# Kernel optimization log

Measured on AMD Instinct MI355X. Metric: run time of the kernel, lower is better.

Reference implementation:

```python
import jax, jax.numpy as jnp
import numpy as np

B, N, D = 16, 512, 256
HEADS = 8
HIDEF = 1024
BLOCK, WINDOW = 32, 64
LEVELS = 5
PYOUT = 128
NCLS, NANCH = 5, 9
NEG = -1e9


def _sinusoidal_pos(n, d):
    # PositionEmbeddingStatic: deterministic sinusoidal table [n, d]
    pos = np.arange(n)[:, None].astype(np.float64)
    i = np.arange(d)[None, :]
    angle = pos / np.power(10000.0, (2 * (i // 2)) / d)
    pe = np.where(i % 2 == 0, np.sin(angle), np.cos(angle))
    return jnp.asarray(pe, jnp.float32)


def _layernorm(x, g, b, eps=1e-5):
    m = x.mean(-1, keepdims=True)
    v = x.var(-1, keepdims=True)
    return (x - m) * jax.lax.rsqrt(v + eps) * g + b


def _bn(x_bcn, g, b, eps=1e-5):
    # BatchNorm1d in training mode: per-channel batch stats over (B, N)
    m = x_bcn.mean((0, 2), keepdims=True)
    v = x_bcn.var((0, 2), keepdims=True)
    return (x_bcn - m) * jax.lax.rsqrt(v + eps) * g[None, :, None] + b[None, :, None]


def _sparse_attention(x, Wqkv, bqkv, Wo, bo):
    # Windowed block-sparse attention: queries in block i attend to key blocks
    # [i-w, i+w] with w = window_size // block_size. Never materializes SxS.
    Bx, Nx, Dx = x.shape
    H, dh = HEADS, Dx // HEADS
    nb, bs = Nx // BLOCK, BLOCK
    w = WINDOW // BLOCK
    qkv = x @ Wqkv + bqkv
    q, k, v = jnp.split(qkv, 3, axis=-1)

    def to_blocks(t):  # [B,N,D] -> [B,H,nb,bs,dh]
        return t.reshape(Bx, nb, bs, H, dh).transpose(0, 3, 1, 2, 4)

    q, k, v = to_blocks(q), to_blocks(k), to_blocks(v)
    offs = list(range(-w, w + 1))
    # roll by -o puts key block (i+o) at query-block position i
    k_band = jnp.concatenate([jnp.roll(k, -o, axis=2) for o in offs], axis=3)
    v_band = jnp.concatenate([jnp.roll(v, -o, axis=2) for o in offs], axis=3)
    blk = jnp.arange(nb)
    valid = jnp.concatenate(
        [jnp.repeat(((blk + o >= 0) & (blk + o < nb))[:, None], bs, axis=1) for o in offs],
        axis=1)  # [nb, (2w+1)*bs]
    scale = 1.0 / jnp.sqrt(jnp.asarray(dh, x.dtype))
    scores = jnp.einsum('bhnqd,bhnkd->bhnqk', q, k_band) * scale
    scores = jnp.where(valid[None, None, :, None, :], scores, NEG)
    p = jax.nn.softmax(scores, axis=-1)
    o = jnp.einsum('bhnqk,bhnkd->bhnqd', p, v_band)
    o = o.transpose(0, 2, 3, 1, 4).reshape(Bx, Nx, Dx)
    return o @ Wo + bo


def setup_inputs():
    key = jax.random.key(0)
    ks = iter(jax.random.split(key, 48))
    g = lambda shape, s=0.02: jax.random.normal(next(ks), shape, jnp.float32) * s
    z = lambda *shape: jnp.zeros(shape, jnp.float32)
    o = lambda *shape: jnp.ones(shape, jnp.float32)
    return {
        'x': jax.random.normal(next(ks), (B, N, D), jnp.float32),
        'patch_W': g((D, D)), 'patch_b': z(D),
        'ln_g': o(D), 'ln_b': z(D),
        'ff_W1': g((D, HIDEF)), 'ff_b1': z(HIDEF),
        'ff_W2': g((HIDEF, D)), 'ff_b2': z(D),
        'Wqkv': g((D, 3 * D)), 'bqkv': z(3 * D),
        'Wo': g((D, D)), 'bo': z(D),
        'bn1_g': o(D), 'bn1_b': z(D),
        'bn2_g': o(D), 'bn2_b': z(D),
        'pyr_W': g((LEVELS, D, PYOUT)), 'pyr_b': z(LEVELS, PYOUT),
        'fcl_W': g((LEVELS * PYOUT * N, 128), 0.005), 'fcl_b': z(128),
        'addbn_g': o(128), 'addbn_b': z(128),
        'cls_W1': g((128, 256)), 'cls_b1': z(256),
        'cls_W2': g((256, NCLS * NANCH)), 'cls_b2': z(NCLS * NANCH),
        'box_W1': g((128, 128)), 'box_b1': z(128),
        'box_W2': g((128, 4 * NANCH)), 'box_b2': z(4 * NANCH),
    }


def reference(x, patch_W, patch_b, ln_g, ln_b, ff_W1, ff_b1, ff_W2, ff_b2,
              Wqkv, bqkv, Wo, bo, bn1_g, bn1_b, bn2_g, bn2_b,
              pyr_W, pyr_b, fcl_W, fcl_b, addbn_g, addbn_b,
              cls_W1, cls_b1, cls_W2, cls_b2, box_W1, box_b1, box_W2, box_b2):
    pos = _sinusoidal_pos(N, D)

    def ff(h):
        return jax.nn.gelu(h @ ff_W1 + ff_b1) @ ff_W2 + ff_b2

    def mnt(h):
        h = _layernorm(h @ patch_W + patch_b, ln_g, ln_b)  # patch embed + norm
        h = h + pos[None]
        idt = h
        h = ff(h)
        h = _sparse_attention(h, Wqkv, bqkv, Wo, bo)
        h = h + idt
        h = _bn(h.transpose(0, 2, 1), bn1_g, bn1_b).transpose(0, 2, 1)
        idt = h
        h = ff(h) + idt
        h = _bn(h.transpose(0, 2, 1), bn2_g, bn2_b).transpose(0, 2, 1)
        return h

    outs = []
    for _ in range(5):
        x = mnt(x)
        outs.append(x.transpose(0, 2, 1))  # [B, D, N]

    # pyramid: per-level 1x1 conv D -> 128
    feats = [jnp.einsum('bdn,dc->bcn', outs[i], pyr_W[i]) + pyr_b[i][None, :, None]
             for i in range(LEVELS)]
    flat = jnp.concatenate([f.reshape(f.shape[0], -1) for f in feats], axis=1)
    add = (flat @ fcl_W + fcl_b)[:, :, None]          # [B,128,1]
    add = _bn(add, addbn_g, addbn_b).transpose(0, 2, 1)  # [B,1,128]
    cls = jax.nn.relu(add @ cls_W1 + cls_b1) @ cls_W2 + cls_b2
    cls = jax.nn.softmax(cls, axis=-1).reshape(-1, NANCH, NCLS)  # eval mode softmax
    box = (jax.nn.relu(add @ box_W1 + box_b1) @ box_W2 + box_b2).reshape(-1, NANCH, 4)
    return jnp.concatenate([cls, box], axis=-1)  # [B, NANCH, NCLS+4]
```

## Files before the change

### kernel.cpp

```cpp
#include <hip/hip_runtime.h>
#include <hip/hip_bf16.h>
#include <math.h>

#define B_ 16
#define N_ 512
#define D_ 256
#define HEADS_ 8
#define DH_ 32
#define HIDEF_ 1024
#define NBLK_ 16
#define BS_ 32
#define LEVELS_ 5
#define PYOUT_ 128
#define ROWS_ (B_ * N_)
#define FCL_K 327680
#define FCL_KB 256
#define FCL_CHUNKS 1280

typedef __attribute__((ext_vector_type(8))) short short8;
typedef __attribute__((ext_vector_type(4))) short short4v;
typedef __attribute__((ext_vector_type(4))) unsigned short ushort4v;
typedef __attribute__((ext_vector_type(4))) float f32x4;

__device__ __forceinline__ float bf2f(short u) {
    return __uint_as_float(((unsigned int)(unsigned short)u) << 16);
}
__device__ __forceinline__ unsigned short f2bf(float x) {
    __hip_bfloat16 h = __float2bfloat16(x);
    return *reinterpret_cast<unsigned short*>(&h);
}

__global__ void pos_kernel(float* __restrict__ pos) {
    int idx = blockIdx.x * 256 + threadIdx.x;
    if (idx >= N_ * D_) return;
    int n = idx >> 8, i = idx & 255;
    double angle = (double)n / pow(10000.0, (double)(2 * (i >> 1)) / 256.0);
    pos[idx] = (float)((i & 1) ? cos(angle) : sin(angle));
}

__device__ __forceinline__ float gelu_f(float x) {
    float x3 = x * x * x;
    return 0.5f * x * (1.f + tanhf(0.7978845608028654f * (x + 0.044715f * x3)));
}

__global__ void tobf16_kernel(const float* __restrict__ x, __hip_bfloat16* __restrict__ y, int n) {
    int i = blockIdx.x * 256 + threadIdx.x;
    if (i < n) y[i] = __float2bfloat16(x[i]);
}

__global__ __launch_bounds__(256) void wconv_kernel(const float* __restrict__ W,
                                                    __hip_bfloat16* __restrict__ Wt,
                                                    int K, int N) {
    int z = blockIdx.z;
    const float* Wz = W + (size_t)z * K * N;
    __hip_bfloat16* Wtz = Wt + (size_t)z * K * N;
    __shared__ float t[32][33];
    int bx = blockIdx.x * 32, by = blockIdx.y * 32;
    int tx = threadIdx.x, ty = threadIdx.y;
#pragma unroll
    for (int i = 0; i < 32; i += 8)
        t[ty + i][tx] = Wz[(size_t)(by + ty + i) * N + bx + tx];
    __syncthreads();
#pragma unroll
    for (int i = 0; i < 32; i += 8)
        Wtz[(size_t)(bx + ty + i) * K + by + tx] = __float2bfloat16(t[tx][ty + i]);
}

template <int ACT, bool OUTF, bool OUTB, bool SCAT, bool STATS, int BN>
__global__ __launch_bounds__(256) void bgemm_kernel(
    const __hip_bfloat16* __restrict__ A, const __hip_bfloat16* __restrict__ Wt,
    const float* __restrict__ bias, const float* __restrict__ resid,
    float* __restrict__ C, __hip_bfloat16* __restrict__ Cb, int M, int Nn, int K,
    int level, float* __restrict__ bnp) {
    __shared__ __hip_bfloat16 Alds[128 * 32];
    __shared__ __hip_bfloat16 Blds[BN * 32];
    constexpr int MW = (BN == 128) ? 4 : 2;
    constexpr int WH = (BN == 128) ? 64 : 32;
    constexpr int BR = BN / 64;
    int tid = threadIdx.x;
    int wid = tid >> 6, lane = tid & 63;
    int row0 = blockIdx.y * 128, col0 = blockIdx.x * BN;
    int wr = (BN == 128) ? (wid >> 1) : wid;
    int wc = (BN == 128) ? (wid & 1) : 0;
    int r16 = lane & 15, kq = lane >> 4;
    int rdoff = kq ^ ((r16 >> 1) & 3);

    f32x4 acc[MW][4];
#pragma unroll
    for (int m = 0; m < MW; m++)
#pragma unroll
        for (int n = 0; n < 4; n++) acc[m][n] = (f32x4){0.f, 0.f, 0.f, 0.f};

    for (int k0 = 0; k0 < K; k0 += 32) {
#pragma unroll
        for (int i = 0; i < 2; i++) {
            int slot = i * 256 + tid;
            int row = slot >> 2, qp = slot & 3;
            int q = qp ^ ((row >> 1) & 3);
            const __hip_bfloat16* ga = A + (size_t)(row0 + row) * K + k0 + q * 8;
            __builtin_amdgcn_global_load_lds(
                (const __attribute__((address_space(1))) void*)ga,
                (__attribute__((address_space(3))) void*)((char*)Alds + i * 4096 + wid * 1024),
                16, 0, 0);
        }
#pragma unroll
        for (int i = 0; i < BR; i++) {
            int slot = i * 256 + tid;
            int row = slot >> 2, qp = slot & 3;
            int q = qp ^ ((row >> 1) & 3);
            const __hip_bfloat16* gb = Wt + (size_t)(col0 + row) * K + k0 + q * 8;
            __builtin_amdgcn_global_load_lds(
                (const __attribute__((address_space(1))) void*)gb,
                (__attribute__((address_space(3))) void*)((char*)Blds + i * 4096 + wid * 1024),
                16, 0, 0);
        }
        __syncthreads();
        short8 af[MW], bf[4];
#pragma unroll
        for (int m = 0; m < MW; m++) {
            int row = wr * WH + m * 16 + r16;
            af[m] = *reinterpret_cast<const short8*>(
                reinterpret_cast<const char*>(Alds) + row * 64 + rdoff * 16);
        }
#pragma unroll
        for (int n = 0; n < 4; n++) {
            int row = wc * 64 + n * 16 + r16;
            bf[n] = *reinterpret_cast<const short8*>(
                reinterpret_cast<const char*>(Blds) + row * 64 + rdoff * 16);
        }
#pragma unroll
        for (int m = 0; m < MW; m++)
#pragma unroll
            for (int n = 0; n < 4; n++)
                acc[m][n] = __builtin_amdgcn_mfma_f32_16x16x32_bf16(af[m], bf[n], acc[m][n], 0, 0, 0);
        __syncthreads();
    }

    int rg = lane >> 4;
    float s1a[4] = {0.f, 0.f, 0.f, 0.f}, s2a[4] = {0.f, 0.f, 0.f, 0.f};
    if (SCAT) {
#pragma unroll
        for (int n = 0; n < 4; n++) {
            int cc = col0 + wc * 64 + n * 16 + r16;
            int bb = cc >> 9, nn = cc & 511;
            float* dst = C + (size_t)bb * (LEVELS_ * PYOUT_ * N_) +
                         (size_t)level * PYOUT_ * N_ + nn;
#pragma unroll
            for (int m = 0; m < MW; m++) {
                int rbase = wr * WH + m * 16 + rg * 4;
#pragma unroll
                for (int j = 0; j < 4; j++) {
                    int ch = rbase + j;
                    dst[(size_t)ch * N_] = acc[m][n][j] + bias[ch];
                }
            }
        }
    } else {
#pragma unroll
        for (int n = 0; n < 4; n++) {
            int cc = col0 + wc * 64 + n * 16 + r16;
            float bv = bias[cc];
#pragma unroll
            for (int m = 0; m < MW; m++) {
                int rb = row0 + wr * WH + m * 16 + rg * 4;
#pragma unroll
                for (int j = 0; j < 4; j++) {
                    int r = rb + j;
                    float v = acc[m][n][j] + bv;
                    if (resid) v += resid[(size_t)r * Nn + cc];
                    if (ACT == 1) v = gelu_f(v);
                    if (OUTF) C[(size_t)r * Nn + cc] = v;
                    if (OUTB) Cb[(size_t)r * Nn + cc] = __float2bfloat16(v);
                    if (STATS) { s1a[n] += v; s2a[n] += v * v; }
                }
            }
        }
    }
    if (STATS) {
        float* sc = (float*)Alds;
        int part = wid * 4 + rg;
#pragma unroll
        for (int n = 0; n < 4; n++) {
            int c = wc * 64 + n * 16 + r16;
            sc[c * 16 + part] = s1a[n];
            sc[1024 + c * 16 + part] = s2a[n];
        }
        __syncthreads();
        if (tid < BN) {
            float a = 0.f, b2 = 0.f;
#pragma unroll
            for (int p = 0; p < 16; p++) {
                a += sc[tid * 16 + p];
                b2 += sc[1024 + tid * 16 + p];
            }
            bnp[blockIdx.y * 256 + col0 + tid] = a;
            bnp[16384 + blockIdx.y * 256 + col0 + tid] = b2;
        }
    }
}

__global__ __launch_bounds__(256) void ln_pos_kernel(
    const float* __restrict__ t, const float* __restrict__ g,
    const float* __restrict__ b, const float* __restrict__ pos,
    float* __restrict__ h, __hip_bfloat16* __restrict__ hb) {
    int lane = threadIdx.x & 63;
    int row = blockIdx.x * 4 + (threadIdx.x >> 6);
    const float4* xr = (const float4*)(t + (size_t)row * D_);
    float4 v = xr[lane];
    float s = v.x + v.y + v.z + v.w;
#pragma unroll
    for (int mk = 32; mk; mk >>= 1) s += __shfl_xor(s, mk);
    float mean = s * (1.f / 256.f);
    float dx = v.x - mean, dy = v.y - mean, dz = v.z - mean, dw = v.w - mean;
    float q = dx * dx + dy * dy + dz * dz + dw * dw;
#pragma unroll
    for (int mk = 32; mk; mk >>= 1) q += __shfl_xor(q, mk);
    float rstd = rsqrtf(q * (1.f / 256.f) + 1e-5f);
    float4 g4 = ((const float4*)g)[lane];
    float4 b4 = ((const float4*)b)[lane];
    float4 p4 = ((const float4*)pos)[(size_t)(row & (N_ - 1)) * 64 + lane];
    float o0 = dx * rstd * g4.x + b4.x + p4.x;
    float o1 = dy * rstd * g4.y + b4.y + p4.y;
    float o2 = dz * rstd * g4.z + b4.z + p4.z;
    float o3 = dw * rstd * g4.w + b4.w + p4.w;
    ((float4*)(h + (size_t)row * D_))[lane] = (float4){o0, o1, o2, o3};
    ushort4v u = {f2bf(o0), f2bf(o1), f2bf(o2), f2bf(o3)};
    *((ushort4v*)(hb + (size_t)row * D_) + lane) = u;
}

__global__ __launch_bounds__(256) void bn_finish_kernel(
    const float* __restrict__ bnp, float* __restrict__ stats) {
    int c = threadIdx.x;
    float s = 0.f, s2 = 0.f;
#pragma unroll 4
    for (int y = 0; y < 64; y++) {
        s += bnp[y * 256 + c];
        s2 += bnp[16384 + y * 256 + c];
    }
    float m = s * (1.f / 8192.f);
    stats[c] = m;
    stats[D_ + c] = s2 * (1.f / 8192.f) - m * m;
}

__global__ __launch_bounds__(256) void bn_apply_kernel(
    const float* __restrict__ x, const float* __restrict__ stats,
    const float* __restrict__ g, const float* __restrict__ b,
    float* __restrict__ y, __hip_bfloat16* __restrict__ yb) {
    int lane = threadIdx.x & 63;
    int row = blockIdx.x * 4 + (threadIdx.x >> 6);
    float4 m4 = ((const float4*)stats)[lane];
    float4 v4 = ((const float4*)(stats + D_))[lane];
    float4 g4 = ((const float4*)g)[lane];
    float4 b4 = ((const float4*)b)[lane];
    float4 x4 = ((const float4*)(x + (size_t)row * D_))[lane];
    float o0 = (x4.x - m4.x) * rsqrtf(v4.x + 1e-5f) * g4.x + b4.x;
    float o1 = (x4.y - m4.y) * rsqrtf(v4.y + 1e-5f) * g4.y + b4.y;
    float o2 = (x4.z - m4.z) * rsqrtf(v4.z + 1e-5f) * g4.z + b4.z;
    float o3 = (x4.w - m4.w) * rsqrtf(v4.w + 1e-5f) * g4.w + b4.w;
    if (y) ((float4*)(y + (size_t)row * D_))[lane] = (float4){o0, o1, o2, o3};
    if (yb) {
        ushort4v u = {f2bf(o0), f2bf(o1), f2bf(o2), f2bf(o3)};
        *((ushort4v*)(yb + (size_t)row * D_) + lane) = u;
    }
}

__global__ __launch_bounds__(256) void attn_kernel(
    const __hip_bfloat16* __restrict__ qkv, __hip_bfloat16* __restrict__ outb) {
    int bx = blockIdx.x, h = blockIdx.y, b = blockIdx.z;
    int tid = threadIdx.x;
    int wid = tid >> 6, lane = tid & 63;
    __shared__ __hip_bfloat16 Klds[256 * 32];
    __shared__ __hip_bfloat16 Vt[32 * 264];
    const short* q16 = (const short*)qkv;

#pragma unroll
    for (int r = 0; r < 4; r++) {
        int slot = r * 256 + tid;
        int row = slot >> 2, qp = slot & 3;
        int ql = qp ^ ((row >> 1) & 3);
        int jb = bx * 4 - 2 + (row >> 5);
        jb = jb < 0 ? 0 : (jb > 15 ? 15 : jb);
        const short* ga = q16 + ((size_t)(b * N_ + jb * 32 + (row & 31))) * 768 + 256 + h * 32 + ql * 8;
        __builtin_amdgcn_global_load_lds(
            (const __attribute__((address_space(1))) void*)ga,
            (__attribute__((address_space(3))) void*)((char*)Klds + r * 4096 + wid * 1024),
            16, 0, 0);
    }
    {
        int row = tid;
        int jb = bx * 4 - 2 + (row >> 5);
        jb = jb < 0 ? 0 : (jb > 15 ? 15 : jb);
        const short* gv = q16 + ((size_t)(b * N_ + jb * 32 + (row & 31))) * 768 + 512 + h * 32;
        short8 v0 = *(const short8*)(gv);
        short8 v1 = *(const short8*)(gv + 8);
        short8 v2 = *(const short8*)(gv + 16);
        short8 v3 = *(const short8*)(gv + 24);
        short* vt = (short*)Vt;
#pragma unroll
        for (int e = 0; e < 8; e++) {
            vt[(e) * 264 + row] = v0[e];
            vt[(8 + e) * 264 + row] = v1[e];
            vt[(16 + e) * 264 + row] = v2[e];
            vt[(24 + e) * 264 + row] = v3[e];
        }
    }
    __syncthreads();

    int i = bx * 4 + wid;
    int c = lane & 15, g = lane >> 4;
    const float scale = 0.17677669529663687f;

#pragma unroll
    for (int qt = 0; qt < 2; qt++) {
        const short* qa = q16 + ((size_t)(b * N_ + i * 32 + qt * 16 + c)) * 768 + h * 32 + g * 8;
        short8 bq = *(const short8*)qa;
        f32x4 st[10];
#pragma unroll
        for (int t = 0; t < 10; t++) {
            int jb = i - 2 + (t >> 1);
            if (jb >= 0 && jb < NBLK_) {
                int row = wid * 32 + t * 16 + c;
                int phys = g ^ ((row >> 1) & 3);
                short8 ak = *(const short8*)((const char*)Klds + row * 64 + phys * 16);
                st[t] = __builtin_amdgcn_mfma_f32_16x16x32_bf16(
                    ak, bq, (f32x4){0.f, 0.f, 0.f, 0.f}, 0, 0, 0);
            }
        }
        float mx = -1e30f;
#pragma unroll
        for (int t = 0; t < 10; t++) {
            int jb = i - 2 + (t >> 1);
            if (jb >= 0 && jb < NBLK_) {
#pragma unroll
                for (int j = 0; j < 4; j++) {
                    st[t][j] *= scale;
                    mx = fmaxf(mx, st[t][j]);
                }
            }
        }
        mx = fmaxf(mx, __shfl_xor(mx, 16));
        mx = fmaxf(mx, __shfl_xor(mx, 32));
        float sum = 0.f;
#pragma unroll
        for (int t = 0; t < 10; t++) {
            int jb = i - 2 + (t >> 1);
            if (jb >= 0 && jb < NBLK_) {
#pragma unroll
                for (int j = 0; j < 4; j++) {
                    float e = __expf(st[t][j] - mx);
                    st[t][j] = e;
                    sum += e;
                }
            }
        }
        sum += __shfl_xor(sum, 16);
        sum += __shfl_xor(sum, 32);
        float inv = 1.f / sum;
        f32x4 o0 = (f32x4){0.f, 0.f, 0.f, 0.f};
        f32x4 o1 = (f32x4){0.f, 0.f, 0.f, 0.f};
        const short* vt = (const short*)Vt;
#pragma unroll
        for (int t = 0; t < 10; t++) {
            int jb = i - 2 + (t >> 1);
            if (jb >= 0 && jb < NBLK_) {
                short8 pa = (short8)0;
#pragma unroll
                for (int j = 0; j < 4; j++) pa[j] = (short)f2bf(st[t][j] * inv);
                int kb = wid * 32 + t * 16 + g * 4;
                short4v vb0 = *(const short4v*)(vt + (0 * 16 + c) * 264 + kb);
                short4v vb1 = *(const short4v*)(vt + (1 * 16 + c) * 264 + kb);
                short8 b0 = (short8)0, b1 = (short8)0;
#pragma unroll
                for (int e = 0; e < 4; e++) { b0[e] = vb0[e]; b1[e] = vb1[e]; }
                o0 = __builtin_amdgcn_mfma_f32_16x16x32_bf16(pa, b0, o0, 0, 0, 0);
                o1 = __builtin_amdgcn_mfma_f32_16x16x32_bf16(pa, b1, o1, 0, 0, 0);
            }
        }
#pragma unroll
        for (int j = 0; j < 4; j++) {
            size_t rbase = ((size_t)(b * N_ + i * 32 + qt * 16 + g * 4 + j)) * D_ + h * DH_;
            outb[rbase + c] = __float2bfloat16(o0[j]);
            outb[rbase + 16 + c] = __float2bfloat16(o1[j]);
        }
    }
}

__global__ __launch_bounds__(256) void fcl_partial_kernel(
    const float* __restrict__ flat, const float* __restrict__ W,
    float* __restrict__ partial) {
    int chunk = blockIdx.x;
    int t = threadIdx.x;
    int k0 = chunk * FCL_KB;
    __shared__ float fl[FCL_KB][18];
#pragma unroll
    for (int b = 0; b < 16; b++)
        fl[t][b] = flat[(size_t)b * FCL_K + k0 + t];
    __syncthreads();
    int jq = t & 31, bg = t >> 5;
    f32x4 acc0 = (f32x4){0.f, 0.f, 0.f, 0.f};
    f32x4 acc1 = (f32x4){0.f, 0.f, 0.f, 0.f};
    const f32x4* W4 = (const f32x4*)W;
#pragma unroll 8
    for (int k = 0; k < FCL_KB; k++) {
        f32x4 wv = W4[(size_t)(k0 + k) * 32 + jq];
        float2 f2 = *(const float2*)&fl[k][bg * 2];
        acc0 += wv * f2.x;
        acc1 += wv * f2.y;
    }
    *(f32x4*)&partial[((size_t)chunk * 16 + bg * 2 + 0) * 128 + jq * 4] = acc0;
    *(f32x4*)&partial[((size_t)chunk * 16 + bg * 2 + 1) * 128 + jq * 4] = acc1;
}

__global__ __launch_bounds__(256) void fcl_reduce_kernel(
    const float* __restrict__ partial, const float* __restrict__ fcl_b,
    float* __restrict__ add) {
    int c0 = blockIdx.x * 32;
    int t = threadIdx.x;
    int ry = t >> 5, cx = t & 31;
    float s = 0.f;
    for (int r = ry; r < FCL_CHUNKS; r += 8)
        s += partial[(size_t)r * 2048 + c0 + cx];
    __shared__ float red[8][32];
    red[ry][cx] = s; __syncthreads();
    if (ry == 0) {
        float tot = 0.f;
#pragma unroll
        for (int q = 0; q < 8; q++) tot += red[q][cx];
        int col = c0 + cx;
        add[col] = tot + fcl_b[col & 127];
    }
}

__global__ __launch_bounds__(256) void head_kernel(
    const float* __restrict__ add, const float* __restrict__ abg, const float* __restrict__ abb,
    const float* __restrict__ cls_W1, const float* __restrict__ cls_b1,
    const float* __restrict__ cls_W2, const float* __restrict__ cls_b2,
    const float* __restrict__ box_W1, const float* __restrict__ box_b1,
    const float* __restrict__ box_W2, const float* __restrict__ box_b2,
    float* __restrict__ out) {
    __shared__ float a2[16][128];
    __shared__ float cm[16][256];
    __shared__ float cls[16][45];
    __shared__ float bmid[16][128];
    __shared__ float smden[16];
    int t = threadIdx.x;
    if (t < 128) {
        float m = 0.f;
#pragma unroll
        for (int b = 0; b < 16; b++) m += add[b * 128 + t];
        m *= (1.f / 16.f);
        float v = 0.f;
#pragma unroll
        for (int b = 0; b < 16; b++) { float d = add[b * 128 + t] - m; v += d * d; }
        v *= (1.f / 16.f);
        float sc = rsqrtf(v + 1e-5f) * abg[t];
#pragma unroll
        for (int b = 0; b < 16; b++) a2[b][t] = (add[b * 128 + t] - m) * sc + abb[t];
    }
    __syncthreads();
    for (int idx = t; idx < 4096; idx += 256) {
        int m = idx >> 8, c = idx & 255;
        float a = cls_b1[c];
        for (int k = 0; k < 128; k++) a += a2[m][k] * cls_W1[k * 256 + c];
        cm[m][c] = fmaxf(a, 0.f);
    }
    for (int idx = t; idx < 2048; idx += 256) {
        int m = idx >> 7, c = idx & 127;
        float a = box_b1[c];
        for (int k = 0; k < 128; k++) a += a2[m][k] * box_W1[k * 128 + c];
        bmid[m][c] = fmaxf(a, 0.f);
    }
    __syncthreads();
    for (int idx = t; idx < 720; idx += 256) {
        int m = idx / 45, c = idx % 45;
        float a = cls_b2[c];
        for (int k = 0; k < 256; k++) a += cm[m][k] * cls_W2[k * 45 + c];
        cls[m][c] = a;
    }
    __syncthreads();
    if (t < 16) {
        float mx = -1e30f;
        for (int c = 0; c < 45; c++) mx = fmaxf(mx, cls[t][c]);
        float s = 0.f;
        for (int c = 0; c < 45; c++) { float e = expf(cls[t][c] - mx); cls[t][c] = e; s += e; }
        smden[t] = s;
    }
    for (int idx = t; idx < 576; idx += 256) {
        int m = idx / 36, c = idx % 36;
        float a = box_b2[c];
        for (int k = 0; k < 128; k++) a += bmid[m][k] * box_W2[k * 36 + c];
        out[m * 81 + (c >> 2) * 9 + 5 + (c & 3)] = a;
    }
    __syncthreads();
    for (int idx = t; idx < 720; idx += 256) {
        int m = idx / 45, c = idx % 45;
        out[m * 81 + (c / 5) * 9 + (c % 5)] = cls[m][c] / smden[m];
    }
}

extern "C" void kernel_launch(void* const* d_in, const int* in_sizes, int n_in,
                              void* d_out, int out_size, void* d_ws, size_t ws_size,
                              hipStream_t stream) {
    const float* x_in    = (const float*)d_in[0];
    const float* patch_W = (const float*)d_in[1];
    const float* patch_b = (const float*)d_in[2];
    const float* ln_g    = (const float*)d_in[3];
    const float* ln_b    = (const float*)d_in[4];
    const float* ff_W1   = (const float*)d_in[5];
    const float* ff_b1   = (const float*)d_in[6];
    const float* ff_W2   = (const float*)d_in[7];
    const float* ff_b2   = (const float*)d_in[8];
    const float* Wqkv    = (const float*)d_in[9];
    const float* bqkv    = (const float*)d_in[10];
    const float* Wo      = (const float*)d_in[11];
    const float* bo      = (const float*)d_in[12];
    const float* bn1_g   = (const float*)d_in[13];
    const float* bn1_b   = (const float*)d_in[14];
    const float* bn2_g   = (const float*)d_in[15];
    const float* bn2_b   = (const float*)d_in[16];
    const float* pyr_W   = (const float*)d_in[17];
    const float* pyr_b   = (const float*)d_in[18];
    const float* fcl_W   = (const float*)d_in[19];
    const float* fcl_b   = (const float*)d_in[20];
    const float* addbn_g = (const float*)d_in[21];
    const float* addbn_b = (const float*)d_in[22];
    const float* cls_W1  = (const float*)d_in[23];
    const float* cls_b1  = (const float*)d_in[24];
    const float* cls_W2  = (const float*)d_in[25];
    const float* cls_b2  = (const float*)d_in[26];
    const float* box_W1  = (const float*)d_in[27];
    const float* box_b1  = (const float*)d_in[28];
    const float* box_W2  = (const float*)d_in[29];
    const float* box_b2  = (const float*)d_in[30];
    float* out = (float*)d_out;

    float* ws = (float*)d_ws;
    size_t off = 0;
    float* POS   = ws + off; off += 131072;
    float* H     = ws + off; off += 2097152;
    float* T     = ws + off; off += 2097152;
    float* UNION = ws + off; off += 4194304;
    float* FLAT  = ws + off; off += 5242880;
    float* PART  = ws + off; off += (size_t)FCL_CHUNKS * 2048;
    float* STATS = ws + off; off += 512;
    float* BNP   = ws + off; off += 2 * 64 * 256;
    float* ADD   = ws + off; off += 2048;
    __hip_bfloat16* Hb   = (__hip_bfloat16*)(ws + off); off += 1048576;
    __hip_bfloat16* Tb   = (__hip_bfloat16*)(ws + off); off += 1048576;
    __hip_bfloat16* Xb   = (__hip_bfloat16*)(ws + off); off += 1048576;
    __hip_bfloat16* ATb  = (__hip_bfloat16*)(ws + off); off += 1048576;
    __hip_bfloat16* patchWt = (__hip_bfloat16*)(ws + off); off += 32768;
    __hip_bfloat16* qkvWt   = (__hip_bfloat16*)(ws + off); off += 98304;
    __hip_bfloat16* WoWt    = (__hip_bfloat16*)(ws + off); off += 32768;
    __hip_bfloat16* W1t     = (__hip_bfloat16*)(ws + off); off += 131072;
    __hip_bfloat16* W2t     = (__hip_bfloat16*)(ws + off); off += 131072;
    __hip_bfloat16* pyrWt   = (__hip_bfloat16*)(ws + off); off += 81920;
    __hip_bfloat16* MIDb = (__hip_bfloat16*)UNION;
    __hip_bfloat16* QKVb = (__hip_bfloat16*)UNION;

    pos_kernel<<<(N_ * D_ + 255) / 256, 256, 0, stream>>>(POS);
    wconv_kernel<<<dim3(D_ / 32, D_ / 32, 1), dim3(32, 8), 0, stream>>>(patch_W, patchWt, D_, D_);
    wconv_kernel<<<dim3(768 / 32, D_ / 32, 1), dim3(32, 8), 0, stream>>>(Wqkv, qkvWt, D_, 768);
    wconv_kernel<<<dim3(D_ / 32, D_ / 32, 1), dim3(32, 8), 0, stream>>>(Wo, WoWt, D_, D_);
    wconv_kernel<<<dim3(HIDEF_ / 32, D_ / 32, 1), dim3(32, 8), 0, stream>>>(ff_W1, W1t, D_, HIDEF_);
    wconv_kernel<<<dim3(D_ / 32, HIDEF_ / 32, 1), dim3(32, 8), 0, stream>>>(ff_W2, W2t, HIDEF_, D_);
    wconv_kernel<<<dim3(PYOUT_ / 32, D_ / 32, LEVELS_), dim3(32, 8), 0, stream>>>(pyr_W, pyrWt, D_, PYOUT_);
    tobf16_kernel<<<(ROWS_ * D_ + 255) / 256, 256, 0, stream>>>(x_in, Xb, ROWS_ * D_);

    for (int it = 0; it < 5; it++) {
        bgemm_kernel<0, true, false, false, false, 64><<<dim3(4, 64), 256, 0, stream>>>(
            Xb, patchWt, patch_b, nullptr, T, nullptr, ROWS_, D_, D_, 0, nullptr);
        ln_pos_kernel<<<ROWS_ / 4, 256, 0, stream>>>(T, ln_g, ln_b, POS, H, Hb);
        bgemm_kernel<1, false, true, false, false, 128><<<dim3(8, 64), 256, 0, stream>>>(
            Hb, W1t, ff_b1, nullptr, nullptr, MIDb, ROWS_, HIDEF_, D_, 0, nullptr);
        bgemm_kernel<0, false, true, false, false, 64><<<dim3(4, 64), 256, 0, stream>>>(
            MIDb, W2t, ff_b2, nullptr, nullptr, Tb, ROWS_, D_, HIDEF_, 0, nullptr);
        bgemm_kernel<0, false, true, false, false, 128><<<dim3(6, 64), 256, 0, stream>>>(
            Tb, qkvWt, bqkv, nullptr, nullptr, QKVb, ROWS_, 768, D_, 0, nullptr);
        attn_kernel<<<dim3(4, HEADS_, B_), 256, 0, stream>>>(QKVb, ATb);
        bgemm_kernel<0, true, false, false, true, 64><<<dim3(4, 64), 256, 0, stream>>>(
            ATb, WoWt, bo, H, T, nullptr, ROWS_, D_, D_, 0, BNP);
        bn_finish_kernel<<<1, 256, 0, stream>>>(BNP, STATS);
        bn_apply_kernel<<<ROWS_ / 4, 256, 0, stream>>>(T, STATS, bn1_g, bn1_b, H, Hb);
        bgemm_kernel<1, false, true, false, false, 128><<<dim3(8, 64), 256, 0, stream>>>(
            Hb, W1t, ff_b1, nullptr, nullptr, MIDb, ROWS_, HIDEF_, D_, 0, nullptr);
        bgemm_kernel<0, true, false, false, true, 64><<<dim3(4, 64), 256, 0, stream>>>(
            MIDb, W2t, ff_b2, H, T, nullptr, ROWS_, D_, HIDEF_, 0, BNP);
        bn_finish_kernel<<<1, 256, 0, stream>>>(BNP, STATS);
        bn_apply_kernel<<<ROWS_ / 4, 256, 0, stream>>>(T, STATS, bn2_g, bn2_b, nullptr, Xb);
        bgemm_kernel<0, false, false, true, false, 64><<<dim3(128, 1), 256, 0, stream>>>(
            pyrWt + (size_t)it * D_ * PYOUT_, Xb, pyr_b + it * PYOUT_, nullptr,
            FLAT, nullptr, PYOUT_, ROWS_, D_, it, nullptr);
    }

    fcl_partial_kernel<<<FCL_CHUNKS, 256, 0, stream>>>(FLAT, fcl_W, PART);
    fcl_reduce_kernel<<<64, 256, 0, stream>>>(PART, fcl_b, ADD);
    head_kernel<<<1, 256, 0, stream>>>(ADD, addbn_g, addbn_b,
        cls_W1, cls_b1, cls_W2, cls_b2, box_W1, box_b1, box_W2, box_b2, out);
    (void)in_sizes; (void)n_in; (void)out_size; (void)ws_size;
}
```

Before: 1.035 ms.

## Fuse patch GEMM with LayerNorm, fold BN finish into apply, retile FCL partial

A new kernel computes the patch-embedding GEMM for 32-row tiles with MFMA, stages the output in LDS, and applies LayerNorm plus the positional add in place. This removes the fp32 round trip of T and one launch per iteration. BN stat finishing is merged into the apply kernel: each of 256 blocks recomputes the column stats from the partials and then normalizes 32 rows, which removes two launches per iteration at the cost of redundant stat reads. The FCL partial kernel is remapped so each thread handles one output column for 8 batches, using scalar weight loads and float4 LDS reads.

```diff
diff --git a/kernel.cpp b/kernel.cpp
--- a/kernel.cpp
+++ b/kernel.cpp
@@ -199,68 +199,144 @@
     }
 }
 
-__global__ __launch_bounds__(256) void ln_pos_kernel(
-    const float* __restrict__ t, const float* __restrict__ g,
-    const float* __restrict__ b, const float* __restrict__ pos,
-    float* __restrict__ h, __hip_bfloat16* __restrict__ hb) {
-    int lane = threadIdx.x & 63;
-    int row = blockIdx.x * 4 + (threadIdx.x >> 6);
-    const float4* xr = (const float4*)(t + (size_t)row * D_);
-    float4 v = xr[lane];
-    float s = v.x + v.y + v.z + v.w;
-#pragma unroll
-    for (int mk = 32; mk; mk >>= 1) s += __shfl_xor(s, mk);
-    float mean = s * (1.f / 256.f);
-    float dx = v.x - mean, dy = v.y - mean, dz = v.z - mean, dw = v.w - mean;
-    float q = dx * dx + dy * dy + dz * dz + dw * dw;
-#pragma unroll
-    for (int mk = 32; mk; mk >>= 1) q += __shfl_xor(q, mk);
-    float rstd = rsqrtf(q * (1.f / 256.f) + 1e-5f);
+__global__ __launch_bounds__(256) void patchln_kernel(
+    const __hip_bfloat16* __restrict__ A, const __hip_bfloat16* __restrict__ Wt,
+    const float* __restrict__ bias, const float* __restrict__ lng,
+    const float* __restrict__ lnb, const float* __restrict__ pos,
+    float* __restrict__ H, __hip_bfloat16* __restrict__ Hb) {
+    __shared__ char __attribute__((aligned(16))) smem[33280];
+    __hip_bfloat16* Alds = (__hip_bfloat16*)smem;
+    __hip_bfloat16* Blds = (__hip_bfloat16*)(smem + 2048);
+    float (*Cls)[260] = (float(*)[260])smem;
+    int tid = threadIdx.x;
+    int wid = tid >> 6, lane = tid & 63;
+    int row0 = blockIdx.x * 32;
+    int r16 = lane & 15, kq = lane >> 4, g = lane >> 4;
+    int rdoff = kq ^ ((r16 >> 1) & 3);
+
+    f32x4 acc[2][4];
+#pragma unroll
+    for (int m = 0; m < 2; m++)
+#pragma unroll
+        for (int n = 0; n < 4; n++) acc[m][n] = (f32x4){0.f, 0.f, 0.f, 0.f};
+
+    for (int k0 = 0; k0 < 256; k0 += 32) {
+        if (tid < 128) {
+            int row = tid >> 2, qp = tid & 3;
+            int q = qp ^ ((row >> 1) & 3);
+            const __hip_bfloat16* ga = A + (size_t)(row0 + row) * 256 + k0 + q * 8;
+            __builtin_amdgcn_global_load_lds(
+                (const __attribute__((address_space(1))) void*)ga,
+                (__attribute__((address_space(3))) void*)((char*)Alds + wid * 1024),
+                16, 0, 0);
+        }
+#pragma unroll
+        for (int i = 0; i < 4; i++) {
+            int slot = i * 256 + tid;
+            int row = slot >> 2, qp = slot & 3;
+            int q = qp ^ ((row >> 1) & 3);
+            const __hip_bfloat16* gb = Wt + (size_t)row * 256 + k0 + q * 8;
+            __builtin_amdgcn_global_load_lds(
+                (const __attribute__((address_space(1))) void*)gb,
+                (__attribute__((address_space(3))) void*)((char*)Blds + i * 4096 + wid * 1024),
+                16, 0, 0);
+        }
+        __syncthreads();
+        short8 af[2], bf[4];
+#pragma unroll
+        for (int m = 0; m < 2; m++) {
+            int row = m * 16 + r16;
+            af[m] = *reinterpret_cast<const short8*>(
+                reinterpret_cast<const char*>(Alds) + row * 64 + rdoff * 16);
+        }
+#pragma unroll
+        for (int n = 0; n < 4; n++) {
+            int row = wid * 64 + n * 16 + r16;
+            bf[n] = *reinterpret_cast<const short8*>(
+                reinterpret_cast<const char*>(Blds) + row * 64 + rdoff * 16);
+        }
+#pragma unroll
+        for (int m = 0; m < 2; m++)
+#pragma unroll
+            for (int n = 0; n < 4; n++)
+                acc[m][n] = __builtin_amdgcn_mfma_f32_16x16x32_bf16(af[m], bf[n], acc[m][n], 0, 0, 0);
+        __syncthreads();
+    }
+#pragma unroll
+    for (int n = 0; n < 4; n++) {
+        int col = wid * 64 + n * 16 + r16;
+        float bv = bias[col];
+#pragma unroll
+        for (int m = 0; m < 2; m++)
+#pragma unroll
+            for (int j = 0; j < 4; j++)
+                Cls[m * 16 + g * 4 + j][col] = acc[m][n][j] + bv;
+    }
+    __syncthreads();
+    float4 g4 = ((const float4*)lng)[lane];
+    float4 b4 = ((const float4*)lnb)[lane];
+#pragma unroll
+    for (int rr = 0; rr < 8; rr++) {
+        int r = wid * 8 + rr;
+        float4 v = *(const float4*)&Cls[r][lane * 4];
+        float s = v.x + v.y + v.z + v.w;
+#pragma unroll
+        for (int mk = 32; mk; mk >>= 1) s += __shfl_xor(s, mk);
+        float mean = s * (1.f / 256.f);
+        float dx = v.x - mean, dy = v.y - mean, dz = v.z - mean, dw = v.w - mean;
+        float q = dx * dx + dy * dy + dz * dz + dw * dw;
+#pragma unroll
+        for (int mk = 32; mk; mk >>= 1) q += __shfl_xor(q, mk);
+        float rstd = rsqrtf(q * (1.f / 256.f) + 1e-5f);
+        int grow = row0 + r;
+        float4 p4 = ((const float4*)pos)[(size_t)(grow & (N_ - 1)) * 64 + lane];
+        float o0 = dx * rstd * g4.x + b4.x + p4.x;
+        float o1 = dy * rstd * g4.y + b4.y + p4.y;
+        float o2 = dz * rstd * g4.z + b4.z + p4.z;
+        float o3 = dw * rstd * g4.w + b4.w + p4.w;
+        ((float4*)(H + (size_t)grow * D_))[lane] = (float4){o0, o1, o2, o3};
+        ushort4v u = {f2bf(o0), f2bf(o1), f2bf(o2), f2bf(o3)};
+        *((ushort4v*)(Hb + (size_t)grow * D_) + lane) = u;
+    }
+}
+
+__global__ __launch_bounds__(256) void bn_applyfin_kernel(
+    const float* __restrict__ x, const float* __restrict__ bnp,
+    const float* __restrict__ g, const float* __restrict__ b,
+    float* __restrict__ y, __hip_bfloat16* __restrict__ yb) {
+    int tid = threadIdx.x;
+    __shared__ float sm[256], sv[256];
+    {
+        float s = 0.f, s2 = 0.f;
+#pragma unroll 4
+        for (int yy = 0; yy < 64; yy++) {
+            s += bnp[yy * 256 + tid];
+            s2 += bnp[16384 + yy * 256 + tid];
+        }
+        float m = s * (1.f / 8192.f);
+        sm[tid] = m;
+        sv[tid] = rsqrtf(s2 * (1.f / 8192.f) - m * m + 1e-5f);
+    }
+    __syncthreads();
+    int lane = tid & 63, w = tid >> 6;
+    int row0 = blockIdx.x * 32;
+    float4 m4 = *(const float4*)&sm[lane * 4];
+    float4 r4 = *(const float4*)&sv[lane * 4];
     float4 g4 = ((const float4*)g)[lane];
     float4 b4 = ((const float4*)b)[lane];
-    float4 p4 = ((const float4*)pos)[(size_t)(row & (N_ - 1)) * 64 + lane];
-    float o0 = dx * rstd * g4.x + b4.x + p4.x;
-    float o1 = dy * rstd * g4.y + b4.y + p4.y;
-    float o2 = dz * rstd * g4.z + b4.z + p4.z;
-    float o3 = dw * rstd * g4.w + b4.w + p4.w;
-    ((float4*)(h + (size_t)row * D_))[lane] = (float4){o0, o1, o2, o3};
-    ushort4v u = {f2bf(o0), f2bf(o1), f2bf(o2), f2bf(o3)};
-    *((ushort4v*)(hb + (size_t)row * D_) + lane) = u;
-}
-
-__global__ __launch_bounds__(256) void bn_finish_kernel(
-    const float* __restrict__ bnp, float* __restrict__ stats) {
-    int c = threadIdx.x;
-    float s = 0.f, s2 = 0.f;
-#pragma unroll 4
-    for (int y = 0; y < 64; y++) {
-        s += bnp[y * 256 + c];
-        s2 += bnp[16384 + y * 256 + c];
-    }
-    float m = s * (1.f / 8192.f);
-    stats[c] = m;
-    stats[D_ + c] = s2 * (1.f / 8192.f) - m * m;
-}
-
-__global__ __launch_bounds__(256) void bn_apply_kernel(
-    const float* __restrict__ x, const float* __restrict__ stats,
-    const float* __restrict__ g, const float* __restrict__ b,
-    float* __restrict__ y, __hip_bfloat16* __restrict__ yb) {
-    int lane = threadIdx.x & 63;
-    int row = blockIdx.x * 4 + (threadIdx.x >> 6);
-    float4 m4 = ((const float4*)stats)[lane];
-    float4 v4 = ((const float4*)(stats + D_))[lane];
-    float4 g4 = ((const float4*)g)[lane];
-    float4 b4 = ((const float4*)b)[lane];
-    float4 x4 = ((const float4*)(x + (size_t)row * D_))[lane];
-    float o0 = (x4.x - m4.x) * rsqrtf(v4.x + 1e-5f) * g4.x + b4.x;
-    float o1 = (x4.y - m4.y) * rsqrtf(v4.y + 1e-5f) * g4.y + b4.y;
-    float o2 = (x4.z - m4.z) * rsqrtf(v4.z + 1e-5f) * g4.z + b4.z;
-    float o3 = (x4.w - m4.w) * rsqrtf(v4.w + 1e-5f) * g4.w + b4.w;
-    if (y) ((float4*)(y + (size_t)row * D_))[lane] = (float4){o0, o1, o2, o3};
-    if (yb) {
-        ushort4v u = {f2bf(o0), f2bf(o1), f2bf(o2), f2bf(o3)};
-        *((ushort4v*)(yb + (size_t)row * D_) + lane) = u;
+#pragma unroll
+    for (int rr = 0; rr < 8; rr++) {
+        int row = row0 + w * 8 + rr;
+        float4 x4 = ((const float4*)(x + (size_t)row * D_))[lane];
+        float o0 = (x4.x - m4.x) * r4.x * g4.x + b4.x;
+        float o1 = (x4.y - m4.y) * r4.y * g4.y + b4.y;
+        float o2 = (x4.z - m4.z) * r4.z * g4.z + b4.z;
+        float o3 = (x4.w - m4.w) * r4.w * g4.w + b4.w;
+        if (y) ((float4*)(y + (size_t)row * D_))[lane] = (float4){o0, o1, o2, o3};
+        if (yb) {
+            ushort4v u = {f2bf(o0), f2bf(o1), f2bf(o2), f2bf(o3)};
+            *((ushort4v*)(yb + (size_t)row * D_) + lane) = u;
+        }
     }
 }
 
@@ -391,24 +467,27 @@
     int chunk = blockIdx.x;
     int t = threadIdx.x;
     int k0 = chunk * FCL_KB;
-    __shared__ float fl[FCL_KB][18];
+    __shared__ float fl[FCL_KB][20];
 #pragma unroll
     for (int b = 0; b < 16; b++)
         fl[t][b] = flat[(size_t)b * FCL_K + k0 + t];
     __syncthreads();
-    int jq = t & 31, bg = t >> 5;
-    f32x4 acc0 = (f32x4){0.f, 0.f, 0.f, 0.f};
-    f32x4 acc1 = (f32x4){0.f, 0.f, 0.f, 0.f};
-    const f32x4* W4 = (const f32x4*)W;
+    int j = t & 127, bg = t >> 7;
+    f32x4 a0 = (f32x4){0.f, 0.f, 0.f, 0.f};
+    f32x4 a1 = (f32x4){0.f, 0.f, 0.f, 0.f};
 #pragma unroll 8
     for (int k = 0; k < FCL_KB; k++) {
-        f32x4 wv = W4[(size_t)(k0 + k) * 32 + jq];
-        float2 f2 = *(const float2*)&fl[k][bg * 2];
-        acc0 += wv * f2.x;
-        acc1 += wv * f2.y;
-    }
-    *(f32x4*)&partial[((size_t)chunk * 16 + bg * 2 + 0) * 128 + jq * 4] = acc0;
-    *(f32x4*)&partial[((size_t)chunk * 16 + bg * 2 + 1) * 128 + jq * 4] = acc1;
+        float w = W[(size_t)(k0 + k) * 128 + j];
+        f32x4 f0 = *(const f32x4*)&fl[k][bg * 8];
+        f32x4 f1 = *(const f32x4*)&fl[k][bg * 8 + 4];
+        a0 += f0 * w;
+        a1 += f1 * w;
+    }
+#pragma unroll
+    for (int bi = 0; bi < 4; bi++) {
+        partial[((size_t)chunk * 16 + bg * 8 + bi) * 128 + j] = a0[bi];
+        partial[((size_t)chunk * 16 + bg * 8 + 4 + bi) * 128 + j] = a1[bi];
+    }
 }
 
 __global__ __launch_bounds__(256) void fcl_reduce_kernel(
@@ -557,6 +636,7 @@
     __hip_bfloat16* pyrWt   = (__hip_bfloat16*)(ws + off); off += 81920;
     __hip_bfloat16* MIDb = (__hip_bfloat16*)UNION;
     __hip_bfloat16* QKVb = (__hip_bfloat16*)UNION;
+    (void)STATS;
 
     pos_kernel<<<(N_ * D_ + 255) / 256, 256, 0, stream>>>(POS);
     wconv_kernel<<<dim3(D_ / 32, D_ / 32, 1), dim3(32, 8), 0, stream>>>(patch_W, patchWt, D_, D_);
@@ -568,9 +648,7 @@
     tobf16_kernel<<<(ROWS_ * D_ + 255) / 256, 256, 0, stream>>>(x_in, Xb, ROWS_ * D_);
 
     for (int it = 0; it < 5; it++) {
-        bgemm_kernel<0, true, false, false, false, 64><<<dim3(4, 64), 256, 0, stream>>>(
-            Xb, patchWt, patch_b, nullptr, T, nullptr, ROWS_, D_, D_, 0, nullptr);
-        ln_pos_kernel<<<ROWS_ / 4, 256, 0, stream>>>(T, ln_g, ln_b, POS, H, Hb);
+        patchln_kernel<<<256, 256, 0, stream>>>(Xb, patchWt, patch_b, ln_g, ln_b, POS, H, Hb);
         bgemm_kernel<1, false, true, false, false, 128><<<dim3(8, 64), 256, 0, stream>>>(
             Hb, W1t, ff_b1, nullptr, nullptr, MIDb, ROWS_, HIDEF_, D_, 0, nullptr);
         bgemm_kernel<0, false, true, false, false, 64><<<dim3(4, 64), 256, 0, stream>>>(
@@ -580,14 +658,12 @@
         attn_kernel<<<dim3(4, HEADS_, B_), 256, 0, stream>>>(QKVb, ATb);
         bgemm_kernel<0, true, false, false, true, 64><<<dim3(4, 64), 256, 0, stream>>>(
             ATb, WoWt, bo, H, T, nullptr, ROWS_, D_, D_, 0, BNP);
-        bn_finish_kernel<<<1, 256, 0, stream>>>(BNP, STATS);
-        bn_apply_kernel<<<ROWS_ / 4, 256, 0, stream>>>(T, STATS, bn1_g, bn1_b, H, Hb);
+        bn_applyfin_kernel<<<256, 256, 0, stream>>>(T, BNP, bn1_g, bn1_b, H, Hb);
         bgemm_kernel<1, false, true, false, false, 128><<<dim3(8, 64), 256, 0, stream>>>(
             Hb, W1t, ff_b1, nullptr, nullptr, MIDb, ROWS_, HIDEF_, D_, 0, nullptr);
         bgemm_kernel<0, true, false, false, true, 64><<<dim3(4, 64), 256, 0, stream>>>(
             MIDb, W2t, ff_b2, H, T, nullptr, ROWS_, D_, HIDEF_, 0, BNP);
-        bn_finish_kernel<<<1, 256, 0, stream>>>(BNP, STATS);
-        bn_apply_kernel<<<ROWS_ / 4, 256, 0, stream>>>(T, STATS, bn2_g, bn2_b, nullptr, Xb);
+        bn_applyfin_kernel<<<256, 256, 0, stream>>>(T, BNP, bn2_g, bn2_b, nullptr, Xb);
         bgemm_kernel<0, false, false, true, false, 64><<<dim3(128, 1), 256, 0, stream>>>(
             pyrWt + (size_t)it * D_ * PYOUT_, Xb, pyr_b + it * PYOUT_, nullptr,
             FLAT, nullptr, PYOUT_, ROWS_, D_, it, nullptr);
```

New measurement: 1.004 ms. 3.0% less time.
